# Kernel tuning notes

Hardware: AMD Instinct MI355X
Metric: run time of the kernel (lower is better)

## Reference

```python
import jax, jax.numpy as jnp
import numpy as np

B, N, C = 2, 2048, 16            # images, proposals/image, classes (incl. background)
IMG_W = IMG_H = 1024.0           # DOTA patch size
SCORE_THRESH = 0.05
NMS_THRESH = 0.5
DET_PER_IMG = 100
BBOX_XFORM_CLIP = float(np.log(1000.0 / 16.0))
WX, WY, WW, WH = 10.0, 10.0, 5.0, 5.0  # BoxCoder weights


def setup_inputs() -> dict:
    key = jax.random.key(0)
    k1, k2, k3, k4 = jax.random.split(key, 4)
    class_logits = jax.random.normal(k1, (B, N, C), dtype=jnp.float32)
    box_regression = jax.random.normal(k2, (B, N, C * 5), dtype=jnp.float32)
    # valid xyxy proposal boxes inside a 1024x1024 image
    xy = jax.random.uniform(k3, (B, N, 2), dtype=jnp.float32) * (IMG_W - 64.0)
    wh = jax.random.uniform(k4, (B, N, 2), dtype=jnp.float32) * 256.0 + 8.0
    proposals = jnp.concatenate([xy, jnp.minimum(xy + wh, IMG_W - 1.0)], axis=-1)
    return {"class_logits": class_logits, "box_regression": box_regression, "proposals": proposals}


def decode(deltas, boxes):
    """deltas [N,C,5] (dx,dy,dw,dh,dtheta), boxes [N,4] xyxy -> ([N,C,4], [N,C])."""
    w = boxes[:, 2] - boxes[:, 0] + 1.0
    h = boxes[:, 3] - boxes[:, 1] + 1.0
    cx = boxes[:, 0] + 0.5 * w
    cy = boxes[:, 1] + 0.5 * h
    dx = deltas[..., 0] / WX
    dy = deltas[..., 1] / WY
    dw = jnp.minimum(deltas[..., 2] / WW, BBOX_XFORM_CLIP)
    dh = jnp.minimum(deltas[..., 3] / WH, BBOX_XFORM_CLIP)
    theta = deltas[..., 4]
    pcx = dx * w[:, None] + cx[:, None]
    pcy = dy * h[:, None] + cy[:, None]
    pw = jnp.exp(dw) * w[:, None]
    ph = jnp.exp(dh) * h[:, None]
    pred = jnp.stack([pcx - 0.5 * pw, pcy - 0.5 * ph,
                      pcx + 0.5 * pw - 1.0, pcy + 0.5 * ph - 1.0], axis=-1)
    return pred, theta


def pairwise_iou(b):
    area = (b[:, 2] - b[:, 0] + 1.0) * (b[:, 3] - b[:, 1] + 1.0)
    lt = jnp.maximum(b[:, None, :2], b[None, :, :2])
    rb = jnp.minimum(b[:, None, 2:], b[None, :, 2:])
    wh = jnp.clip(rb - lt + 1.0, 0.0)
    inter = wh[..., 0] * wh[..., 1]
    return inter / (area[:, None] + area[None, :] - inter)


def nms_class(boxes, scores, theta):
    """Greedy NMS for one class. Returns score-sorted boxes/scores/theta + keep mask."""
    valid = scores > SCORE_THRESH
    order = jnp.argsort(-scores)
    sb, ss, st, sv = boxes[order], scores[order], theta[order], valid[order]
    iou = pairwise_iou(sb)  # [N,N] -- dominant memory traffic

    def step(suppressed, i):
        keep_i = sv[i] & ~suppressed[i]
        suppressed = suppressed | (keep_i & (iou[i] > NMS_THRESH))
        return suppressed, keep_i

    _, keep = jax.lax.scan(step, jnp.zeros((N,), dtype=bool), jnp.arange(N))
    return sb, ss, st, keep


def process_image(logits, deltas, prop_boxes):
    probs = jax.nn.softmax(logits, axis=-1)                 # [N,C]
    boxes, theta = decode(deltas.reshape(N, C, 5), prop_boxes)
    # clip_to_image(remove_empty=False)
    boxes = jnp.stack([jnp.clip(boxes[..., 0], 0.0, IMG_W - 1.0),
                       jnp.clip(boxes[..., 1], 0.0, IMG_H - 1.0),
                       jnp.clip(boxes[..., 2], 0.0, IMG_W - 1.0),
                       jnp.clip(boxes[..., 3], 0.0, IMG_H - 1.0)], axis=-1)
    # skip background class 0; vmap NMS over the C-1 foreground classes
    cb = jnp.transpose(boxes[:, 1:, :], (1, 0, 2))          # [C-1,N,4]
    cs = probs[:, 1:].T                                     # [C-1,N]
    ct = theta[:, 1:].T                                     # [C-1,N]
    sb, ss, st, keep = jax.vmap(nms_class)(cb, cs, ct)
    labels = jnp.broadcast_to(jnp.arange(1, C, dtype=jnp.int32)[:, None], (C - 1, N))
    # keep top detections_per_img by score across all classes (kthvalue filter)
    flat = jnp.where(keep, ss, -1.0).reshape(-1)
    top_s, idx = jax.lax.top_k(flat, DET_PER_IMG)
    valid = top_s > 0.0
    out_boxes = jnp.where(valid[:, None], sb.reshape(-1, 4)[idx], 0.0)
    out_scores = jnp.where(valid, top_s, 0.0)
    out_theta = jnp.where(valid, st.reshape(-1)[idx], 0.0)
    out_labels = jnp.where(valid, labels.reshape(-1)[idx], 0)
    return out_boxes, out_scores, out_theta, out_labels, valid


def reference(class_logits, box_regression, proposals):
    # Returns padded per-image results: boxes [B,D,4], scores [B,D], theta [B,D],
    # labels [B,D] int32, valid mask [B,D].
    return jax.vmap(process_image)(class_logits, box_regression, proposals)
```

## Files before the change

### kernel.cpp

```cpp
#include <hip/hip_runtime.h>

#define NB 2
#define NN 2048
#define NC 16
#define NFG 15
#define NPAIR (NB * NFG)
#define DETS 100
#define TH1 512
#define TKEEP 256
#define SCORE_TH 0.05f
#define NMS_TH 0.5f
#define BBOX_CLIP 4.135166556742356f
#define IMG_MAX 1023.0f

typedef unsigned long long ull;

__device__ __forceinline__ float iou_box(float4 a, float aarea, float4 c) {
    float xx1 = fmaxf(a.x, c.x);
    float yy1 = fmaxf(a.y, c.y);
    float xx2 = fminf(a.z, c.z);
    float yy2 = fminf(a.w, c.w);
    float iw = fmaxf(__fadd_rn(__fsub_rn(xx2, xx1), 1.0f), 0.0f);
    float ih = fmaxf(__fadd_rn(__fsub_rn(yy2, yy1), 1.0f), 0.0f);
    float inter = __fmul_rn(iw, ih);
    float carea = __fmul_rn(__fadd_rn(__fsub_rn(c.z, c.x), 1.0f),
                            __fadd_rn(__fsub_rn(c.w, c.y), 1.0f));
    float denom = __fsub_rn(__fadd_rn(aarea, carea), inter);
    return __fdiv_rn(inter, denom);
}

__device__ __forceinline__ void bitonic2048(ull* keys, int tid) {
    ull r[4];
#pragma unroll
    for (int p = 0; p < 4; ++p) r[p] = keys[tid + p * TH1];

#pragma unroll
    for (unsigned k = 2; k <= 64; k <<= 1) {
        for (unsigned j = k >> 1; j >= 1; j >>= 1) {
#pragma unroll
            for (int p = 0; p < 4; ++p) {
                ull v = __shfl_xor(r[p], (int)j);
                unsigned i = (unsigned)tid + (unsigned)p * TH1;
                bool keepMax = ((((unsigned)tid & j) == 0u) == ((i & k) == 0u));
                bool agtv = r[p] > v;
                r[p] = (agtv == keepMax) ? r[p] : v;
            }
        }
    }
#pragma unroll
    for (int p = 0; p < 4; ++p) keys[tid + p * TH1] = r[p];

    for (unsigned k = 128; k <= 2048; k <<= 1) {
        for (unsigned j = k >> 1; j >= 64; j >>= 1) {
            __syncthreads();
            for (unsigned i = tid; i < NN; i += TH1) {
                unsigned ixj = i ^ j;
                if (ixj > i) {
                    ull a = keys[i], c = keys[ixj];
                    bool sw = ((i & k) == 0) ? (a < c) : (a > c);
                    if (sw) { keys[i] = c; keys[ixj] = a; }
                }
            }
        }
        __syncthreads();
#pragma unroll
        for (int p = 0; p < 4; ++p) r[p] = keys[tid + p * TH1];
        for (unsigned j = 32; j >= 1; j >>= 1) {
#pragma unroll
            for (int p = 0; p < 4; ++p) {
                ull v = __shfl_xor(r[p], (int)j);
                unsigned i = (unsigned)tid + (unsigned)p * TH1;
                bool keepMax = ((((unsigned)tid & j) == 0u) == ((i & k) == 0u));
                bool agtv = r[p] > v;
                r[p] = (agtv == keepMax) ? r[p] : v;
            }
        }
#pragma unroll
        for (int p = 0; p < 4; ++p) keys[tid + p * TH1] = r[p];
    }
    __syncthreads();
}

__global__ __launch_bounds__(256)
void score_kernel(const float* __restrict__ logits,
                  float* __restrict__ scoreAll)
{
    const int g = blockIdx.x * 256 + threadIdx.x;
    const int b = g >> 11;
    const int n = g & (NN - 1);

    const float* lr = logits + (size_t)(b * NN + n) * NC;
    float l[NC];
#pragma unroll
    for (int t = 0; t < NC / 4; ++t) {
        float4 v = ((const float4*)lr)[t];
        l[4*t+0] = v.x; l[4*t+1] = v.y; l[4*t+2] = v.z; l[4*t+3] = v.w;
    }
    float m = l[0];
#pragma unroll
    for (int c = 1; c < NC; ++c) m = fmaxf(m, l[c]);
    float e[NC];
    float sum = 0.0f;
#pragma unroll
    for (int c = 0; c < NC; ++c) {
        e[c] = expf(__fsub_rn(l[c], m));
        sum = __fadd_rn(sum, e[c]);
    }
#pragma unroll
    for (int cf = 0; cf < NFG; ++cf) {
        scoreAll[(size_t)(b * NFG + cf) * NN + n] = __fdiv_rn(e[cf + 1], sum);
    }
}

__global__ __launch_bounds__(TH1)
void nms_kernel(const float* __restrict__ scoreAll,
                const float* __restrict__ deltas,
                const float* __restrict__ props,
                ull*   __restrict__ cKey,
                float* __restrict__ cBox,
                float* __restrict__ cTheta)
{
    const int pair = blockIdx.x;
    const int b    = pair / NFG;
    const int cls  = pair % NFG + 1;
    const int tid  = threadIdx.x;
    const int lane = tid & 63;

    const float* D = deltas + (size_t)b * NN * NC * 5;
    const float* P = props  + (size_t)b * NN * 4;
    const float* S = scoreAll + (size_t)pair * NN;

    __shared__ ull keys[NN];
    __shared__ float4 sbl[NN];
    __shared__ ull supmat[TKEEP][4];
    __shared__ ull remW[NN/64];
    __shared__ int keptPos[DETS];
    __shared__ int keptCnt;

    for (int n = tid; n < NN; n += TH1) {
        float sc = S[n];
        keys[n] = ((ull)__float_as_uint(sc) << 32) | (unsigned)(NN - 1 - n);
    }
    __syncthreads();

    bitonic2048(keys, tid);

    for (int n = tid; n < NN; n += TH1) {
        float sc = __uint_as_float((unsigned)(keys[n] >> 32));
        ull bm = __ballot(sc > SCORE_TH);
        if (lane == 0) remW[n >> 6] = bm;
    }

    for (int n = tid; n < TKEEP; n += TH1) {
        ull key = keys[n];
        int orig = NN - 1 - (int)(key & 0xFFFFFFFFull);

        float4 pv = ((const float4*)P)[orig];
        float w  = __fadd_rn(__fsub_rn(pv.z, pv.x), 1.0f);
        float h  = __fadd_rn(__fsub_rn(pv.w, pv.y), 1.0f);
        float cx = __fadd_rn(pv.x, __fmul_rn(0.5f, w));
        float cy = __fadd_rn(pv.y, __fmul_rn(0.5f, h));

        const float* dd = D + (size_t)orig * NC * 5 + cls * 5;
        float dx = __fdiv_rn(dd[0], 10.0f);
        float dy = __fdiv_rn(dd[1], 10.0f);
        float dw = fminf(__fdiv_rn(dd[2], 5.0f), BBOX_CLIP);
        float dh = fminf(__fdiv_rn(dd[3], 5.0f), BBOX_CLIP);

        float pcx = __fadd_rn(__fmul_rn(dx, w), cx);
        float pcy = __fadd_rn(__fmul_rn(dy, h), cy);
        float pw  = __fmul_rn(expf(dw), w);
        float ph  = __fmul_rn(expf(dh), h);

        float bx1 = __fsub_rn(pcx, __fmul_rn(0.5f, pw));
        float by1 = __fsub_rn(pcy, __fmul_rn(0.5f, ph));
        float bx2 = __fsub_rn(__fadd_rn(pcx, __fmul_rn(0.5f, pw)), 1.0f);
        float by2 = __fsub_rn(__fadd_rn(pcy, __fmul_rn(0.5f, ph)), 1.0f);

        bx1 = fminf(fmaxf(bx1, 0.0f), IMG_MAX);
        by1 = fminf(fmaxf(by1, 0.0f), IMG_MAX);
        bx2 = fminf(fmaxf(bx2, 0.0f), IMG_MAX);
        by2 = fminf(fmaxf(by2, 0.0f), IMG_MAX);

        sbl[n] = make_float4(bx1, by1, bx2, by2);
    }
    __syncthreads();

    for (int t = tid; t < TKEEP * 4; t += TH1) {
        int i = t >> 2, w = t & 3;
        float4 a = sbl[i];
        float aarea = __fmul_rn(__fadd_rn(__fsub_rn(a.z, a.x), 1.0f),
                                __fadd_rn(__fsub_rn(a.w, a.y), 1.0f));
        ull m = 0ull;
#pragma unroll 8
        for (int l = 0; l < 64; ++l) {
            float iou = iou_box(a, aarea, sbl[(w << 6) + l]);
            if (iou > NMS_TH) m |= (1ull << l);
        }
        supmat[i][w] = m;
    }
    __syncthreads();

    if (tid < 64) {
        ull rem = (lane < TKEEP / 64) ? remW[lane] : 0ull;
        int kept = 0;
        while (kept < DETS) {
            ull has = __ballot(rem != 0ull);
            if (has == 0ull) break;
            int fw = (int)__builtin_ctzll(has);
            unsigned lo = (unsigned)__shfl((int)(unsigned)rem, fw);
            unsigned hi = (unsigned)__shfl((int)(unsigned)(rem >> 32), fw);
            ull w64 = ((ull)hi << 32) | lo;
            int i = (fw << 6) + (int)__builtin_ctzll(w64);
            if (lane == 0) keptPos[kept] = i;
            ++kept;
            if (lane < TKEEP / 64) rem &= ~supmat[i][lane];
        }
        if (lane == 0) keptCnt = kept;
    }
    __syncthreads();

    int keptNow = keptCnt;
    if (keptNow < DETS) {
        for (int n = TKEEP + tid; n < NN; n += TH1) {
            ull key = keys[n];
            int orig = NN - 1 - (int)(key & 0xFFFFFFFFull);
            float4 pv = ((const float4*)P)[orig];
            float w  = __fadd_rn(__fsub_rn(pv.z, pv.x), 1.0f);
            float h  = __fadd_rn(__fsub_rn(pv.w, pv.y), 1.0f);
            float cx = __fadd_rn(pv.x, __fmul_rn(0.5f, w));
            float cy = __fadd_rn(pv.y, __fmul_rn(0.5f, h));
            const float* dd = D + (size_t)orig * NC * 5 + cls * 5;
            float dx = __fdiv_rn(dd[0], 10.0f);
            float dy = __fdiv_rn(dd[1], 10.0f);
            float dw = fminf(__fdiv_rn(dd[2], 5.0f), BBOX_CLIP);
            float dh = fminf(__fdiv_rn(dd[3], 5.0f), BBOX_CLIP);
            float pcx = __fadd_rn(__fmul_rn(dx, w), cx);
            float pcy = __fadd_rn(__fmul_rn(dy, h), cy);
            float pw  = __fmul_rn(expf(dw), w);
            float ph  = __fmul_rn(expf(dh), h);
            float bx1 = __fsub_rn(pcx, __fmul_rn(0.5f, pw));
            float by1 = __fsub_rn(pcy, __fmul_rn(0.5f, ph));
            float bx2 = __fsub_rn(__fadd_rn(pcx, __fmul_rn(0.5f, pw)), 1.0f);
            float by2 = __fsub_rn(__fadd_rn(pcy, __fmul_rn(0.5f, ph)), 1.0f);
            bx1 = fminf(fmaxf(bx1, 0.0f), IMG_MAX);
            by1 = fminf(fmaxf(by1, 0.0f), IMG_MAX);
            bx2 = fminf(fmaxf(bx2, 0.0f), IMG_MAX);
            by2 = fminf(fmaxf(by2, 0.0f), IMG_MAX);
            sbl[n] = make_float4(bx1, by1, bx2, by2);
        }
        if (tid < TKEEP / 64) remW[tid] = 0ull;
        __syncthreads();
        for (int k = 0; k < NN / TH1; ++k) {
            int j = k * TH1 + tid;
            bool sup = false;
            if (j >= TKEEP) {
                float4 c = sbl[j];
                for (int q = 0; q < keptNow; ++q) {
                    float4 a = sbl[keptPos[q]];
                    float aarea = __fmul_rn(__fadd_rn(__fsub_rn(a.z, a.x), 1.0f),
                                            __fadd_rn(__fsub_rn(a.w, a.y), 1.0f));
                    sup = sup || (iou_box(a, aarea, c) > NMS_TH);
                }
            }
            ull bm = __ballot(sup);
            if (lane == 0) remW[k * (TH1/64) + (tid >> 6)] &= ~bm;
        }
        __syncthreads();
        int kept = keptNow;
        while (kept < DETS) {
            ull mine = (lane < NN / 64) ? remW[lane] : 0ull;
            ull has = __ballot(mine != 0ull);
            if (has == 0ull) break;
            int fw = (int)__builtin_ctzll(has);
            unsigned lo = (unsigned)__shfl((int)(unsigned)mine, fw);
            unsigned hi = (unsigned)__shfl((int)(unsigned)(mine >> 32), fw);
            ull w64 = ((ull)hi << 32) | lo;
            int i = (fw << 6) + (int)__builtin_ctzll(w64);
            if (tid == 0) keptPos[kept] = i;
            ++kept;
            __syncthreads();
            float4 a = sbl[i];
            float aarea = __fmul_rn(__fadd_rn(__fsub_rn(a.z, a.x), 1.0f),
                                    __fadd_rn(__fsub_rn(a.w, a.y), 1.0f));
#pragma unroll
            for (int k = 0; k < NN / TH1; ++k) {
                int j = k * TH1 + tid;
                float iou = iou_box(a, aarea, sbl[j]);
                ull bm = __ballot(iou > NMS_TH);
                if (lane == 0) remW[k * (TH1/64) + (tid >> 6)] &= ~bm;
            }
            __syncthreads();
        }
        if (tid == 0) keptCnt = kept;
        __syncthreads();
    }

    if (tid < DETS) {
        int kc = keptCnt;
        float sc = -1.0f, th = 0.0f;
        float4 bx = make_float4(0.f, 0.f, 0.f, 0.f);
        if (tid < kc) {
            int p = keptPos[tid];
            ull key = keys[p];
            sc = __uint_as_float((unsigned)(key >> 32));
            bx = sbl[p];
            int orig = NN - 1 - (int)(key & 0xFFFFFFFFull);
            th = D[(size_t)orig * NC * 5 + cls * 5 + 4];
        }
        int g = pair * DETS + tid;
        unsigned vb = __float_as_uint(sc);
        vb = (vb & 0x80000000u) ? ~vb : (vb | 0x80000000u);
        cKey[g] = ((ull)vb << 32)
                | (unsigned)(NN - 1 - ((pair % NFG) * DETS + tid));
        cTheta[g] = th;
        ((float4*)cBox)[g] = bx;
    }
}

__global__ __launch_bounds__(TH1)
void topk_kernel(const ull* __restrict__ cKey,
                 const float* __restrict__ cBox,
                 const float* __restrict__ cTheta,
                 float* __restrict__ out)
{
    const int b   = blockIdx.x;
    const int tid = threadIdx.x;
    const int M   = NFG * DETS;

    __shared__ ull keys[NN];

    const ull* src = cKey + (size_t)b * M;
    for (int t = tid; t < NN; t += TH1)
        keys[t] = (t < M) ? src[t] : 0ull;
    __syncthreads();

    bitonic2048(keys, tid);

    if (tid < DETS) {
        ull key = keys[tid];
        unsigned vb = (unsigned)(key >> 32);
        float val = __uint_as_float((vb & 0x80000000u) ? (vb & 0x7FFFFFFFu) : ~vb);
        bool vld = (key != 0ull) && (val > 0.0f);
        float4 bx = make_float4(0.f, 0.f, 0.f, 0.f);
        float th = 0.f, lab = 0.f, scv = 0.f;
        if (vld) {
            int slot = NN - 1 - (int)(key & 0xFFFFFFFFull);
            size_t g = (size_t)b * M + slot;
            bx  = ((const float4*)cBox)[g];
            th  = cTheta[g];
            lab = (float)(slot / DETS + 1);
            scv = val;
        }
        int o = b * DETS + tid;
        out[o * 4 + 0] = bx.x;
        out[o * 4 + 1] = bx.y;
        out[o * 4 + 2] = bx.z;
        out[o * 4 + 3] = bx.w;
        out[NB * DETS * 4 + o] = scv;
        out[NB * DETS * 5 + o] = th;
        out[NB * DETS * 6 + o] = lab;
        out[NB * DETS * 7 + o] = vld ? 1.0f : 0.0f;
    }
}

extern "C" void kernel_launch(void* const* d_in, const int* in_sizes, int n_in,
                              void* d_out, int out_size, void* d_ws, size_t ws_size,
                              hipStream_t stream) {
    const float* logits = (const float*)d_in[0];
    const float* deltas = (const float*)d_in[1];
    const float* props  = (const float*)d_in[2];
    float* out = (float*)d_out;
    char* ws = (char*)d_ws;

    ull*   cKey     = (ull*)ws;
    float* cBox     = (float*)(ws + sizeof(ull) * NPAIR * DETS);
    float* cTheta   = cBox + (size_t)NPAIR * DETS * 4;
    float* scoreAll = cTheta + (size_t)NPAIR * DETS;

    hipLaunchKernelGGL(score_kernel, dim3(NB * NN / 256), dim3(256), 0, stream,
                       logits, scoreAll);
    hipLaunchKernelGGL(nms_kernel, dim3(NPAIR), dim3(TH1), 0, stream,
                       scoreAll, deltas, props, cKey, cBox, cTheta);
    hipLaunchKernelGGL(topk_kernel, dim3(NB), dim3(TH1), 0, stream,
                       cKey, cBox, cTheta, out);
}
```

Baseline: 132.0 us.

## Fuse score, NMS and top-k kernels into one cooperative kernel

Merges the softmax-score, per-class NMS and cross-class top-k kernels into a single cooperative launch of 30 blocks, separated by grid-wide syncs. This removes two kernel launches and the gaps between them. The suppression matrix in shared memory is also transposed to [4][TKEEP], which changes the bank access pattern for the build and the greedy scan. The trade-off is grid.sync overhead, plus most blocks sitting idle during the score and top-k phases.

```diff
diff --git a/kernel.cpp b/kernel.cpp
--- a/kernel.cpp
+++ b/kernel.cpp
@@ -1,4 +1,7 @@
 #include <hip/hip_runtime.h>
+#include <hip/hip_cooperative_groups.h>
+
+namespace cg = cooperative_groups;
 
 #define NB 2
 #define NN 2048
@@ -81,286 +84,287 @@
     __syncthreads();
 }
 
-__global__ __launch_bounds__(256)
-void score_kernel(const float* __restrict__ logits,
-                  float* __restrict__ scoreAll)
+__global__ __launch_bounds__(TH1)
+void fused_kernel(const float* __restrict__ logits,
+                  const float* __restrict__ deltas,
+                  const float* __restrict__ props,
+                  float* __restrict__ out,
+                  float* __restrict__ scoreAll,
+                  ull*   __restrict__ cKey,
+                  float* __restrict__ cBox,
+                  float* __restrict__ cTheta)
 {
-    const int g = blockIdx.x * 256 + threadIdx.x;
-    const int b = g >> 11;
-    const int n = g & (NN - 1);
-
-    const float* lr = logits + (size_t)(b * NN + n) * NC;
-    float l[NC];
-#pragma unroll
-    for (int t = 0; t < NC / 4; ++t) {
-        float4 v = ((const float4*)lr)[t];
-        l[4*t+0] = v.x; l[4*t+1] = v.y; l[4*t+2] = v.z; l[4*t+3] = v.w;
-    }
-    float m = l[0];
-#pragma unroll
-    for (int c = 1; c < NC; ++c) m = fmaxf(m, l[c]);
-    float e[NC];
-    float sum = 0.0f;
-#pragma unroll
-    for (int c = 0; c < NC; ++c) {
-        e[c] = expf(__fsub_rn(l[c], m));
-        sum = __fadd_rn(sum, e[c]);
-    }
-#pragma unroll
-    for (int cf = 0; cf < NFG; ++cf) {
-        scoreAll[(size_t)(b * NFG + cf) * NN + n] = __fdiv_rn(e[cf + 1], sum);
-    }
-}
-
-__global__ __launch_bounds__(TH1)
-void nms_kernel(const float* __restrict__ scoreAll,
-                const float* __restrict__ deltas,
-                const float* __restrict__ props,
-                ull*   __restrict__ cKey,
-                float* __restrict__ cBox,
-                float* __restrict__ cTheta)
-{
-    const int pair = blockIdx.x;
-    const int b    = pair / NFG;
-    const int cls  = pair % NFG + 1;
+    cg::grid_group grid = cg::this_grid();
+    const int bid  = blockIdx.x;
     const int tid  = threadIdx.x;
     const int lane = tid & 63;
 
-    const float* D = deltas + (size_t)b * NN * NC * 5;
-    const float* P = props  + (size_t)b * NN * 4;
-    const float* S = scoreAll + (size_t)pair * NN;
-
     __shared__ ull keys[NN];
     __shared__ float4 sbl[NN];
-    __shared__ ull supmat[TKEEP][4];
+    __shared__ ull supmat[4][TKEEP];
     __shared__ ull remW[NN/64];
     __shared__ int keptPos[DETS];
     __shared__ int keptCnt;
 
-    for (int n = tid; n < NN; n += TH1) {
-        float sc = S[n];
-        keys[n] = ((ull)__float_as_uint(sc) << 32) | (unsigned)(NN - 1 - n);
-    }
-    __syncthreads();
-
-    bitonic2048(keys, tid);
-
-    for (int n = tid; n < NN; n += TH1) {
-        float sc = __uint_as_float((unsigned)(keys[n] >> 32));
-        ull bm = __ballot(sc > SCORE_TH);
-        if (lane == 0) remW[n >> 6] = bm;
-    }
-
-    for (int n = tid; n < TKEEP; n += TH1) {
-        ull key = keys[n];
-        int orig = NN - 1 - (int)(key & 0xFFFFFFFFull);
-
-        float4 pv = ((const float4*)P)[orig];
-        float w  = __fadd_rn(__fsub_rn(pv.z, pv.x), 1.0f);
-        float h  = __fadd_rn(__fsub_rn(pv.w, pv.y), 1.0f);
-        float cx = __fadd_rn(pv.x, __fmul_rn(0.5f, w));
-        float cy = __fadd_rn(pv.y, __fmul_rn(0.5f, h));
-
-        const float* dd = D + (size_t)orig * NC * 5 + cls * 5;
-        float dx = __fdiv_rn(dd[0], 10.0f);
-        float dy = __fdiv_rn(dd[1], 10.0f);
-        float dw = fminf(__fdiv_rn(dd[2], 5.0f), BBOX_CLIP);
-        float dh = fminf(__fdiv_rn(dd[3], 5.0f), BBOX_CLIP);
-
-        float pcx = __fadd_rn(__fmul_rn(dx, w), cx);
-        float pcy = __fadd_rn(__fmul_rn(dy, h), cy);
-        float pw  = __fmul_rn(expf(dw), w);
-        float ph  = __fmul_rn(expf(dh), h);
-
-        float bx1 = __fsub_rn(pcx, __fmul_rn(0.5f, pw));
-        float by1 = __fsub_rn(pcy, __fmul_rn(0.5f, ph));
-        float bx2 = __fsub_rn(__fadd_rn(pcx, __fmul_rn(0.5f, pw)), 1.0f);
-        float by2 = __fsub_rn(__fadd_rn(pcy, __fmul_rn(0.5f, ph)), 1.0f);
-
-        bx1 = fminf(fmaxf(bx1, 0.0f), IMG_MAX);
-        by1 = fminf(fmaxf(by1, 0.0f), IMG_MAX);
-        bx2 = fminf(fmaxf(bx2, 0.0f), IMG_MAX);
-        by2 = fminf(fmaxf(by2, 0.0f), IMG_MAX);
-
-        sbl[n] = make_float4(bx1, by1, bx2, by2);
-    }
-    __syncthreads();
-
-    for (int t = tid; t < TKEEP * 4; t += TH1) {
-        int i = t >> 2, w = t & 3;
-        float4 a = sbl[i];
-        float aarea = __fmul_rn(__fadd_rn(__fsub_rn(a.z, a.x), 1.0f),
-                                __fadd_rn(__fsub_rn(a.w, a.y), 1.0f));
-        ull m = 0ull;
-#pragma unroll 8
-        for (int l = 0; l < 64; ++l) {
-            float iou = iou_box(a, aarea, sbl[(w << 6) + l]);
-            if (iou > NMS_TH) m |= (1ull << l);
-        }
-        supmat[i][w] = m;
-    }
-    __syncthreads();
-
-    if (tid < 64) {
-        ull rem = (lane < TKEEP / 64) ? remW[lane] : 0ull;
-        int kept = 0;
-        while (kept < DETS) {
-            ull has = __ballot(rem != 0ull);
-            if (has == 0ull) break;
-            int fw = (int)__builtin_ctzll(has);
-            unsigned lo = (unsigned)__shfl((int)(unsigned)rem, fw);
-            unsigned hi = (unsigned)__shfl((int)(unsigned)(rem >> 32), fw);
-            ull w64 = ((ull)hi << 32) | lo;
-            int i = (fw << 6) + (int)__builtin_ctzll(w64);
-            if (lane == 0) keptPos[kept] = i;
-            ++kept;
-            if (lane < TKEEP / 64) rem &= ~supmat[i][lane];
-        }
-        if (lane == 0) keptCnt = kept;
-    }
-    __syncthreads();
-
-    int keptNow = keptCnt;
-    if (keptNow < DETS) {
-        for (int n = TKEEP + tid; n < NN; n += TH1) {
+    {
+        const int g = bid * TH1 + tid;
+        if (g < NB * NN) {
+            const int b = g >> 11;
+            const int n = g & (NN - 1);
+            const float* lr = logits + (size_t)(b * NN + n) * NC;
+            float l[NC];
+#pragma unroll
+            for (int t = 0; t < NC / 4; ++t) {
+                float4 v = ((const float4*)lr)[t];
+                l[4*t+0] = v.x; l[4*t+1] = v.y; l[4*t+2] = v.z; l[4*t+3] = v.w;
+            }
+            float m = l[0];
+#pragma unroll
+            for (int c = 1; c < NC; ++c) m = fmaxf(m, l[c]);
+            float e[NC];
+            float sum = 0.0f;
+#pragma unroll
+            for (int c = 0; c < NC; ++c) {
+                e[c] = expf(__fsub_rn(l[c], m));
+                sum = __fadd_rn(sum, e[c]);
+            }
+#pragma unroll
+            for (int cf = 0; cf < NFG; ++cf) {
+                scoreAll[(size_t)(b * NFG + cf) * NN + n] = __fdiv_rn(e[cf + 1], sum);
+            }
+        }
+    }
+    grid.sync();
+
+    if (bid < NPAIR) {
+        const int pair = bid;
+        const int b    = pair / NFG;
+        const int cls  = pair % NFG + 1;
+
+        const float* D = deltas + (size_t)b * NN * NC * 5;
+        const float* P = props  + (size_t)b * NN * 4;
+        const float* S = scoreAll + (size_t)pair * NN;
+
+        for (int n = tid; n < NN; n += TH1) {
+            float sc = S[n];
+            keys[n] = ((ull)__float_as_uint(sc) << 32) | (unsigned)(NN - 1 - n);
+        }
+        __syncthreads();
+
+        bitonic2048(keys, tid);
+
+        for (int n = tid; n < NN; n += TH1) {
+            float sc = __uint_as_float((unsigned)(keys[n] >> 32));
+            ull bm = __ballot(sc > SCORE_TH);
+            if (lane == 0) remW[n >> 6] = bm;
+        }
+
+        for (int n = tid; n < TKEEP; n += TH1) {
             ull key = keys[n];
             int orig = NN - 1 - (int)(key & 0xFFFFFFFFull);
+
             float4 pv = ((const float4*)P)[orig];
             float w  = __fadd_rn(__fsub_rn(pv.z, pv.x), 1.0f);
             float h  = __fadd_rn(__fsub_rn(pv.w, pv.y), 1.0f);
             float cx = __fadd_rn(pv.x, __fmul_rn(0.5f, w));
             float cy = __fadd_rn(pv.y, __fmul_rn(0.5f, h));
+
             const float* dd = D + (size_t)orig * NC * 5 + cls * 5;
             float dx = __fdiv_rn(dd[0], 10.0f);
             float dy = __fdiv_rn(dd[1], 10.0f);
             float dw = fminf(__fdiv_rn(dd[2], 5.0f), BBOX_CLIP);
             float dh = fminf(__fdiv_rn(dd[3], 5.0f), BBOX_CLIP);
+
             float pcx = __fadd_rn(__fmul_rn(dx, w), cx);
             float pcy = __fadd_rn(__fmul_rn(dy, h), cy);
             float pw  = __fmul_rn(expf(dw), w);
             float ph  = __fmul_rn(expf(dh), h);
+
             float bx1 = __fsub_rn(pcx, __fmul_rn(0.5f, pw));
             float by1 = __fsub_rn(pcy, __fmul_rn(0.5f, ph));
             float bx2 = __fsub_rn(__fadd_rn(pcx, __fmul_rn(0.5f, pw)), 1.0f);
             float by2 = __fsub_rn(__fadd_rn(pcy, __fmul_rn(0.5f, ph)), 1.0f);
+
             bx1 = fminf(fmaxf(bx1, 0.0f), IMG_MAX);
             by1 = fminf(fmaxf(by1, 0.0f), IMG_MAX);
             bx2 = fminf(fmaxf(bx2, 0.0f), IMG_MAX);
             by2 = fminf(fmaxf(by2, 0.0f), IMG_MAX);
+
             sbl[n] = make_float4(bx1, by1, bx2, by2);
         }
-        if (tid < TKEEP / 64) remW[tid] = 0ull;
-        __syncthreads();
-        for (int k = 0; k < NN / TH1; ++k) {
-            int j = k * TH1 + tid;
-            bool sup = false;
-            if (j >= TKEEP) {
-                float4 c = sbl[j];
-                for (int q = 0; q < keptNow; ++q) {
-                    float4 a = sbl[keptPos[q]];
-                    float aarea = __fmul_rn(__fadd_rn(__fsub_rn(a.z, a.x), 1.0f),
-                                            __fadd_rn(__fsub_rn(a.w, a.y), 1.0f));
-                    sup = sup || (iou_box(a, aarea, c) > NMS_TH);
-                }
-            }
-            ull bm = __ballot(sup);
-            if (lane == 0) remW[k * (TH1/64) + (tid >> 6)] &= ~bm;
-        }
-        __syncthreads();
-        int kept = keptNow;
-        while (kept < DETS) {
-            ull mine = (lane < NN / 64) ? remW[lane] : 0ull;
-            ull has = __ballot(mine != 0ull);
-            if (has == 0ull) break;
-            int fw = (int)__builtin_ctzll(has);
-            unsigned lo = (unsigned)__shfl((int)(unsigned)mine, fw);
-            unsigned hi = (unsigned)__shfl((int)(unsigned)(mine >> 32), fw);
-            ull w64 = ((ull)hi << 32) | lo;
-            int i = (fw << 6) + (int)__builtin_ctzll(w64);
-            if (tid == 0) keptPos[kept] = i;
-            ++kept;
-            __syncthreads();
+        __syncthreads();
+
+        for (int p = 0; p < (TKEEP * 4) / TH1; ++p) {
+            int item = p * TH1 + tid;
+            int i = item & (TKEEP - 1);
+            int w = item >> 8;
             float4 a = sbl[i];
             float aarea = __fmul_rn(__fadd_rn(__fsub_rn(a.z, a.x), 1.0f),
                                     __fadd_rn(__fsub_rn(a.w, a.y), 1.0f));
-#pragma unroll
+            ull m = 0ull;
+#pragma unroll 8
+            for (int l = 0; l < 64; ++l) {
+                float iou = iou_box(a, aarea, sbl[(w << 6) + l]);
+                if (iou > NMS_TH) m |= (1ull << l);
+            }
+            supmat[w][i] = m;
+        }
+        __syncthreads();
+
+        if (tid < 64) {
+            ull rem = (lane < TKEEP / 64) ? remW[lane] : 0ull;
+            int kept = 0;
+            while (kept < DETS) {
+                ull has = __ballot(rem != 0ull);
+                if (has == 0ull) break;
+                int fw = (int)__builtin_ctzll(has);
+                unsigned lo = (unsigned)__shfl((int)(unsigned)rem, fw);
+                unsigned hi = (unsigned)__shfl((int)(unsigned)(rem >> 32), fw);
+                ull w64 = ((ull)hi << 32) | lo;
+                int i = (fw << 6) + (int)__builtin_ctzll(w64);
+                if (lane == 0) keptPos[kept] = i;
+                ++kept;
+                if (lane < TKEEP / 64) rem &= ~supmat[lane][i];
+            }
+            if (lane == 0) keptCnt = kept;
+        }
+        __syncthreads();
+
+        int keptNow = keptCnt;
+        if (keptNow < DETS) {
+            for (int n = TKEEP + tid; n < NN; n += TH1) {
+                ull key = keys[n];
+                int orig = NN - 1 - (int)(key & 0xFFFFFFFFull);
+                float4 pv = ((const float4*)P)[orig];
+                float w  = __fadd_rn(__fsub_rn(pv.z, pv.x), 1.0f);
+                float h  = __fadd_rn(__fsub_rn(pv.w, pv.y), 1.0f);
+                float cx = __fadd_rn(pv.x, __fmul_rn(0.5f, w));
+                float cy = __fadd_rn(pv.y, __fmul_rn(0.5f, h));
+                const float* dd = D + (size_t)orig * NC * 5 + cls * 5;
+                float dx = __fdiv_rn(dd[0], 10.0f);
+                float dy = __fdiv_rn(dd[1], 10.0f);
+                float dw = fminf(__fdiv_rn(dd[2], 5.0f), BBOX_CLIP);
+                float dh = fminf(__fdiv_rn(dd[3], 5.0f), BBOX_CLIP);
+                float pcx = __fadd_rn(__fmul_rn(dx, w), cx);
+                float pcy = __fadd_rn(__fmul_rn(dy, h), cy);
+                float pw  = __fmul_rn(expf(dw), w);
+                float ph  = __fmul_rn(expf(dh), h);
+                float bx1 = __fsub_rn(pcx, __fmul_rn(0.5f, pw));
+                float by1 = __fsub_rn(pcy, __fmul_rn(0.5f, ph));
+                float bx2 = __fsub_rn(__fadd_rn(pcx, __fmul_rn(0.5f, pw)), 1.0f);
+                float by2 = __fsub_rn(__fadd_rn(pcy, __fmul_rn(0.5f, ph)), 1.0f);
+                bx1 = fminf(fmaxf(bx1, 0.0f), IMG_MAX);
+                by1 = fminf(fmaxf(by1, 0.0f), IMG_MAX);
+                bx2 = fminf(fmaxf(bx2, 0.0f), IMG_MAX);
+                by2 = fminf(fmaxf(by2, 0.0f), IMG_MAX);
+                sbl[n] = make_float4(bx1, by1, bx2, by2);
+            }
+            if (tid < TKEEP / 64) remW[tid] = 0ull;
+            __syncthreads();
             for (int k = 0; k < NN / TH1; ++k) {
                 int j = k * TH1 + tid;
-                float iou = iou_box(a, aarea, sbl[j]);
-                ull bm = __ballot(iou > NMS_TH);
+                bool sup = false;
+                if (j >= TKEEP) {
+                    float4 c = sbl[j];
+                    for (int q = 0; q < keptNow; ++q) {
+                        float4 a = sbl[keptPos[q]];
+                        float aarea = __fmul_rn(__fadd_rn(__fsub_rn(a.z, a.x), 1.0f),
+                                                __fadd_rn(__fsub_rn(a.w, a.y), 1.0f));
+                        sup = sup || (iou_box(a, aarea, c) > NMS_TH);
+                    }
+                }
+                ull bm = __ballot(sup);
                 if (lane == 0) remW[k * (TH1/64) + (tid >> 6)] &= ~bm;
             }
             __syncthreads();
-        }
-        if (tid == 0) keptCnt = kept;
-        __syncthreads();
-    }
-
-    if (tid < DETS) {
-        int kc = keptCnt;
-        float sc = -1.0f, th = 0.0f;
-        float4 bx = make_float4(0.f, 0.f, 0.f, 0.f);
-        if (tid < kc) {
-            int p = keptPos[tid];
-            ull key = keys[p];
-            sc = __uint_as_float((unsigned)(key >> 32));
-            bx = sbl[p];
-            int orig = NN - 1 - (int)(key & 0xFFFFFFFFull);
-            th = D[(size_t)orig * NC * 5 + cls * 5 + 4];
-        }
-        int g = pair * DETS + tid;
-        unsigned vb = __float_as_uint(sc);
-        vb = (vb & 0x80000000u) ? ~vb : (vb | 0x80000000u);
-        cKey[g] = ((ull)vb << 32)
-                | (unsigned)(NN - 1 - ((pair % NFG) * DETS + tid));
-        cTheta[g] = th;
-        ((float4*)cBox)[g] = bx;
-    }
-}
-
-__global__ __launch_bounds__(TH1)
-void topk_kernel(const ull* __restrict__ cKey,
-                 const float* __restrict__ cBox,
-                 const float* __restrict__ cTheta,
-                 float* __restrict__ out)
-{
-    const int b   = blockIdx.x;
-    const int tid = threadIdx.x;
-    const int M   = NFG * DETS;
-
-    __shared__ ull keys[NN];
-
-    const ull* src = cKey + (size_t)b * M;
-    for (int t = tid; t < NN; t += TH1)
-        keys[t] = (t < M) ? src[t] : 0ull;
-    __syncthreads();
-
-    bitonic2048(keys, tid);
-
-    if (tid < DETS) {
-        ull key = keys[tid];
-        unsigned vb = (unsigned)(key >> 32);
-        float val = __uint_as_float((vb & 0x80000000u) ? (vb & 0x7FFFFFFFu) : ~vb);
-        bool vld = (key != 0ull) && (val > 0.0f);
-        float4 bx = make_float4(0.f, 0.f, 0.f, 0.f);
-        float th = 0.f, lab = 0.f, scv = 0.f;
-        if (vld) {
-            int slot = NN - 1 - (int)(key & 0xFFFFFFFFull);
-            size_t g = (size_t)b * M + slot;
-            bx  = ((const float4*)cBox)[g];
-            th  = cTheta[g];
-            lab = (float)(slot / DETS + 1);
-            scv = val;
-        }
-        int o = b * DETS + tid;
-        out[o * 4 + 0] = bx.x;
-        out[o * 4 + 1] = bx.y;
-        out[o * 4 + 2] = bx.z;
-        out[o * 4 + 3] = bx.w;
-        out[NB * DETS * 4 + o] = scv;
-        out[NB * DETS * 5 + o] = th;
-        out[NB * DETS * 6 + o] = lab;
-        out[NB * DETS * 7 + o] = vld ? 1.0f : 0.0f;
+            int kept = keptNow;
+            while (kept < DETS) {
+                ull mine = (lane < NN / 64) ? remW[lane] : 0ull;
+                ull has = __ballot(mine != 0ull);
+                if (has == 0ull) break;
+                int fw = (int)__builtin_ctzll(has);
+                unsigned lo = (unsigned)__shfl((int)(unsigned)mine, fw);
+                unsigned hi = (unsigned)__shfl((int)(unsigned)(mine >> 32), fw);
+                ull w64 = ((ull)hi << 32) | lo;
+                int i = (fw << 6) + (int)__builtin_ctzll(w64);
+                if (tid == 0) keptPos[kept] = i;
+                ++kept;
+                __syncthreads();
+                float4 a = sbl[i];
+                float aarea = __fmul_rn(__fadd_rn(__fsub_rn(a.z, a.x), 1.0f),
+                                        __fadd_rn(__fsub_rn(a.w, a.y), 1.0f));
+#pragma unroll
+                for (int k = 0; k < NN / TH1; ++k) {
+                    int j = k * TH1 + tid;
+                    float iou = iou_box(a, aarea, sbl[j]);
+                    ull bm = __ballot(iou > NMS_TH);
+                    if (lane == 0) remW[k * (TH1/64) + (tid >> 6)] &= ~bm;
+                }
+                __syncthreads();
+            }
+            if (tid == 0) keptCnt = kept;
+            __syncthreads();
+        }
+
+        if (tid < DETS) {
+            int kc = keptCnt;
+            float sc = -1.0f, th = 0.0f;
+            float4 bx = make_float4(0.f, 0.f, 0.f, 0.f);
+            if (tid < kc) {
+                int p = keptPos[tid];
+                ull key = keys[p];
+                sc = __uint_as_float((unsigned)(key >> 32));
+                bx = sbl[p];
+                int orig = NN - 1 - (int)(key & 0xFFFFFFFFull);
+                th = D[(size_t)orig * NC * 5 + cls * 5 + 4];
+            }
+            int g = pair * DETS + tid;
+            unsigned vb = __float_as_uint(sc);
+            vb = (vb & 0x80000000u) ? ~vb : (vb | 0x80000000u);
+            cKey[g] = ((ull)vb << 32)
+                    | (unsigned)(NN - 1 - ((pair % NFG) * DETS + tid));
+            cTheta[g] = th;
+            ((float4*)cBox)[g] = bx;
+        }
+    }
+    grid.sync();
+
+    if (bid < NB) {
+        const int b = bid;
+        const int M = NFG * DETS;
+
+        const ull* src = cKey + (size_t)b * M;
+        for (int t = tid; t < NN; t += TH1)
+            keys[t] = (t < M) ? src[t] : 0ull;
+        __syncthreads();
+
+        bitonic2048(keys, tid);
+
+        if (tid < DETS) {
+            ull key = keys[tid];
+            unsigned vb = (unsigned)(key >> 32);
+            float val = __uint_as_float((vb & 0x80000000u) ? (vb & 0x7FFFFFFFu) : ~vb);
+            bool vld = (key != 0ull) && (val > 0.0f);
+            float4 bx = make_float4(0.f, 0.f, 0.f, 0.f);
+            float th = 0.f, lab = 0.f, scv = 0.f;
+            if (vld) {
+                int slot = NN - 1 - (int)(key & 0xFFFFFFFFull);
+                size_t g = (size_t)b * M + slot;
+                bx  = ((const float4*)cBox)[g];
+                th  = cTheta[g];
+                lab = (float)(slot / DETS + 1);
+                scv = val;
+            }
+            int o = b * DETS + tid;
+            out[o * 4 + 0] = bx.x;
+            out[o * 4 + 1] = bx.y;
+            out[o * 4 + 2] = bx.z;
+            out[o * 4 + 3] = bx.w;
+            out[NB * DETS * 4 + o] = scv;
+            out[NB * DETS * 5 + o] = th;
+            out[NB * DETS * 6 + o] = lab;
+            out[NB * DETS * 7 + o] = vld ? 1.0f : 0.0f;
+        }
     }
 }
 
@@ -378,10 +382,8 @@
     float* cTheta   = cBox + (size_t)NPAIR * DETS * 4;
     float* scoreAll = cTheta + (size_t)NPAIR * DETS;
 
-    hipLaunchKernelGGL(score_kernel, dim3(NB * NN / 256), dim3(256), 0, stream,
-                       logits, scoreAll);
-    hipLaunchKernelGGL(nms_kernel, dim3(NPAIR), dim3(TH1), 0, stream,
-                       scoreAll, deltas, props, cKey, cBox, cTheta);
-    hipLaunchKernelGGL(topk_kernel, dim3(NB), dim3(TH1), 0, stream,
-                       cKey, cBox, cTheta, out);
+    void* args[] = { (void*)&logits, (void*)&deltas, (void*)&props, (void*)&out,
+                     (void*)&scoreAll, (void*)&cKey, (void*)&cBox, (void*)&cTheta };
+    hipLaunchCooperativeKernel((const void*)fused_kernel, dim3(NPAIR), dim3(TH1),
+                               args, 0, stream);
 }
```

Result: slower. 157.1 us (+19.0%).
